# Optimization experiments

Measured on AMD Instinct MI355X. Metric: run time of the kernel, lower is better.

The kernel has to match this reference:

```python
import jax, jax.numpy as jnp
import numpy as np

B, N_L, N_T, C_IN, HID, NG, ATOMS, N_EDGES = 8, 128, 512, 128, 128, 10, 24, 4096
BN_EPS = 1e-5


def setup_inputs() -> dict:
    key = jax.random.key(0)
    ks = jax.random.split(key, 20)
    f32 = jnp.float32
    s = 0.05  # weight scale
    return {
        "h_l_x": jax.random.normal(ks[0], (B, N_L, C_IN), f32),
        "h_t_x": jax.random.normal(ks[1], (B, N_T, C_IN), f32),
        "l_mask": jnp.ones((B, N_L), dtype=bool),
        "t_mask": jnp.ones((B, N_T), dtype=bool),
        "h_l_pos": jax.random.normal(ks[2], (B, N_L, 3), f32),
        "h_t_pos": jax.random.normal(ks[3], (B, N_T * ATOMS, 3), f32),
        "x_l_flat": jax.random.normal(ks[4], (B * N_L, C_IN), f32),
        "edge_index": jax.random.randint(ks[5], (2, N_EDGES), 0, B * N_L),
        "W1": jax.random.normal(ks[6], (2 * C_IN, HID), f32) * s,
        "b1": jnp.zeros((HID,), f32),
        "bn_gamma": jnp.ones((HID,), f32),
        "bn_beta": jnp.zeros((HID,), f32),
        "bn_mean": jnp.zeros((HID,), f32),
        "bn_var": jnp.ones((HID,), f32),
        "W_pi": jax.random.normal(ks[7], (HID, NG), f32) * s,
        "b_pi": jnp.zeros((NG,), f32),
        "W_sigma": jax.random.normal(ks[8], (HID, NG), f32) * s,
        "b_sigma": jnp.zeros((NG,), f32),
        "W_mu": jax.random.normal(ks[9], (HID, NG), f32) * s,
        "b_mu": jnp.zeros((NG,), f32),
        "W_nuc": jax.random.normal(ks[10], (C_IN, 12), f32) * s,
        "b_nuc": jnp.zeros((12,), f32),
        "W_bond": jax.random.normal(ks[11], (2 * C_IN, 4), f32) * s,
        "b_bond": jnp.zeros((4,), f32),
    }


def reference(h_l_x, h_t_x, l_mask, t_mask, h_l_pos, h_t_pos, x_l_flat, edge_index,
              W1, b1, bn_gamma, bn_beta, bn_mean, bn_var,
              W_pi, b_pi, W_sigma, b_sigma, W_mu, b_mu,
              W_nuc, b_nuc, W_bond, b_bond):
    Bsz, Nl, Cd = h_l_x.shape
    Nt = h_t_x.shape[1]
    # dense pairwise concat: [B, N_l, N_t, 2C] (masks are all-True, so the
    # boolean selection C[C_mask] of the original is a static flatten)
    pair = jnp.concatenate([
        jnp.broadcast_to(h_l_x[:, :, None, :], (Bsz, Nl, Nt, Cd)),
        jnp.broadcast_to(h_t_x[:, None, :, :], (Bsz, Nl, Nt, Cd)),
    ], axis=-1).reshape(-1, 2 * Cd)
    # MLP: Linear -> BatchNorm1d (eval, running stats) -> ELU -> Dropout(eval=id)
    h = pair @ W1 + b1
    h = (h - bn_mean) * jax.lax.rsqrt(bn_var + BN_EPS) * bn_gamma + bn_beta
    h = jax.nn.elu(h)
    # MDN heads
    pi = jax.nn.softmax(h @ W_pi + b_pi, axis=-1)
    sigma = jax.nn.elu(h @ W_sigma + b_sigma) + 1.1
    mu = jax.nn.elu(h @ W_mu + b_mu) + 1.0
    # auxiliary heads on flat ligand node features
    nuc_types = x_l_flat @ W_nuc + b_nuc
    bond_feat = jnp.concatenate([x_l_flat[edge_index[0]], x_l_flat[edge_index[1]]], axis=1)
    bond_types = bond_feat @ W_bond + b_bond
    # pairwise distances with windowed min over 24 atoms per target residue
    d2 = (-2.0 * jnp.einsum('bld,btd->blt', h_l_pos, h_t_pos)
          + jnp.sum(h_t_pos ** 2, axis=-1)[:, None, :]
          + jnp.sum(h_l_pos ** 2, axis=-1)[:, :, None])
    d = jnp.nan_to_num(jnp.sqrt(d2), nan=10000.0)  # nan from sqrt(<0)
    dist = d.reshape(Bsz, Nl, Nt, ATOMS).min(axis=-1)  # [B, N_l, N_t]
    dist = jax.lax.stop_gradient(dist.reshape(-1)[:, None])  # detached, [M,1]
    C_batch = jnp.broadcast_to(jnp.arange(Bsz)[:, None, None], (Bsz, Nl, Nt)).reshape(-1)
    return (pi, sigma, mu, dist, nuc_types, bond_types, C_batch)
```

## Files before the change

### kernel.cpp

```cpp
#include <hip/hip_runtime.h>

#define B_      8
#define N_L     128
#define N_T     512
#define C_IN    128
#define HID     128
#define NG      10
#define ATOMS   24
#define N_EDGES 4096

#define OFF_PI  0
#define OFF_SG  5242880
#define OFF_MU  10485760
#define OFF_DI  15728640
#define OFF_NU  16252928
#define OFF_BO  16265216
#define OFF_CB  16281600

#define WS_U    0
#define WS_V    131072
#define WS_B    659456
#define WS_WT   659488

typedef unsigned short u16;
typedef unsigned int   u32;
typedef short s16x8 __attribute__((ext_vector_type(8)));
typedef float f32x4 __attribute__((ext_vector_type(4)));
typedef u32   u32x4 __attribute__((ext_vector_type(4)));

__device__ __forceinline__ float bfu2f(u16 s) {
  u32 u = ((u32)s) << 16;
  return __builtin_bit_cast(float, u);
}
__device__ __forceinline__ u16 f2bf(float f) {
  u32 u = __builtin_bit_cast(u32, f);
  u32 r = (u + 0x7fffu + ((u >> 16) & 1u)) >> 16;
  return (u16)r;
}
__device__ __forceinline__ u32 pack2(float a, float b) {
  return (u32)f2bf(a) | ((u32)f2bf(b) << 16);
}
__device__ __forceinline__ u32 pkhi(float hi, float lo) {
  return __builtin_amdgcn_perm(__builtin_bit_cast(u32, hi),
                               __builtin_bit_cast(u32, lo), 0x07060302u);
}
__device__ __forceinline__ float eluf(float x) {
  return x > 0.f ? x : __expf(x) - 1.f;
}
__device__ __forceinline__ s16x8 ld8(const u16* p) {
  return __builtin_bit_cast(s16x8, *(const u32x4*)p);
}

template<bool F32>
__device__ __forceinline__ float ldf(const void* p, size_t i) {
  if constexpr (F32) return ((const float*)p)[i];
  else               return bfu2f(((const u16*)p)[i]);
}
template<bool F32>
__device__ __forceinline__ u16 wraw(const void* p, size_t i) {
  if constexpr (F32) return f2bf(((const float*)p)[i]);
  else               return ((const u16*)p)[i];
}
__device__ __forceinline__ bool is_f32(const u32* probe) {
  return (probe[0] & 0xFFFFu) == 0u;
}

template<bool F32>
__device__ __forceinline__ void prep_rows(
    int blk, int tid,
    const void* hlx, const void* htx, const void* W1, const void* b1,
    const void* gam, const void* bet, const void* mean_, const void* var_,
    float* __restrict__ ws, float (*xs)[C_IN]) {
  int k = tid & 127, g = tid >> 7;
  bool isU = (blk < 128);
  const void* x = isU ? hlx : htx;
  int row0 = isU ? blk * 8 : (blk - 128) * 8;
  size_t woff = isU ? 0 : (size_t)C_IN * HID;
  #pragma unroll
  for (int i = 0; i < 4; ++i) {
    int e = tid + i * 256;
    int rr = e >> 7, cc = e & 127;
    xs[rr][cc] = ldf<F32>(x, (size_t)(row0 + rr) * C_IN + cc);
  }
  __syncthreads();
  float a0 = 0.f, a1 = 0.f, a2 = 0.f, a3 = 0.f;
  const float* xr0 = xs[g * 4 + 0];
  const float* xr1 = xs[g * 4 + 1];
  const float* xr2 = xs[g * 4 + 2];
  const float* xr3 = xs[g * 4 + 3];
  #pragma unroll 8
  for (int c = 0; c < C_IN; ++c) {
    float w = ldf<F32>(W1, woff + (size_t)c * HID + k);
    a0 += xr0[c] * w;
    a1 += xr1[c] * w;
    a2 += xr2[c] * w;
    a3 += xr3[c] * w;
  }
  float A = ldf<F32>(gam, k) * rsqrtf(ldf<F32>(var_, k) + 1e-5f);
  float add = 0.f;
  if (isU) add = ldf<F32>(b1, k) * A + (ldf<F32>(bet, k) - ldf<F32>(mean_, k) * A);
  float* dst = ws + (isU ? WS_U : WS_V) + (size_t)row0 * HID;
  dst[(g * 4 + 0) * HID + k] = a0 * A + add;
  dst[(g * 4 + 1) * HID + k] = a1 * A + add;
  dst[(g * 4 + 2) * HID + k] = a2 * A + add;
  dst[(g * 4 + 3) * HID + k] = a3 * A + add;
}

template<bool F32>
__device__ __forceinline__ void prep_consts(
    int tid, const void* Wpi, const void* bpi, const void* Wsg, const void* bsg,
    const void* Wmu, const void* bmu, float* __restrict__ ws) {
  if (tid >= 128) return;
  int k = tid;
  u16* wt = (u16*)(ws + WS_WT);
  for (int j = 0; j < 32; ++j) {
    u16 val = 0;
    if (j < 10)      val = wraw<F32>(Wpi, (size_t)k * NG + j);
    else if (j < 20) val = wraw<F32>(Wsg, (size_t)k * NG + j - 10);
    else if (j < 30) val = wraw<F32>(Wmu, (size_t)k * NG + j - 20);
    wt[(size_t)j * HID + k] = val;
  }
  if (k < 32) {
    float bb = 0.f;
    if (k < 10)      bb = ldf<F32>(bpi, k);
    else if (k < 20) bb = ldf<F32>(bsg, k - 10);
    else if (k < 30) bb = ldf<F32>(bmu, k - 20);
    ws[WS_B + k] = bb;
  }
}

template<bool F32>
__device__ __forceinline__ void dist_impl(int blk2,
                                          const void* __restrict__ lpos,
                                          const void* __restrict__ tpos,
                                          void* __restrict__ out) {
  int lc   = blk2 & 63;
  int half = (blk2 >> 6) & 1;
  int b    = blk2 >> 7;
  int t = half * 256 + threadIdx.x;

  size_t tbase = ((size_t)b * (N_T * ATOMS) + (size_t)t * ATOMS) * 3;
  float ax[ATOMS], ay[ATOMS], az[ATOMS], an[ATOMS];
  if constexpr (F32) {
    float c[72];
    const float4* tp4 = (const float4*)((const float*)tpos + tbase);
    #pragma unroll
    for (int i = 0; i < 18; ++i) {
      float4 qv = tp4[i];
      c[4*i+0] = qv.x; c[4*i+1] = qv.y; c[4*i+2] = qv.z; c[4*i+3] = qv.w;
    }
    #pragma unroll
    for (int a = 0; a < ATOMS; ++a) {
      ax[a] = c[3*a]; ay[a] = c[3*a+1]; az[a] = c[3*a+2];
      an[a] = ax[a]*ax[a] + ay[a]*ay[a] + az[a]*az[a];
    }
  } else {
    u32 raw[36];
    const uint4* tp4 = (const uint4*)((const u16*)tpos + tbase);
    #pragma unroll
    for (int i = 0; i < 9; ++i) {
      uint4 qv = tp4[i];
      raw[4*i+0] = qv.x; raw[4*i+1] = qv.y; raw[4*i+2] = qv.z; raw[4*i+3] = qv.w;
    }
    #pragma unroll
    for (int a = 0; a < ATOMS; ++a) {
      int e = 3 * a;
      u32 w0 = raw[e >> 1];
      ax[a] = bfu2f((e & 1) ? (u16)(w0 >> 16) : (u16)w0);
      u32 w1 = raw[(e + 1) >> 1];
      ay[a] = bfu2f(((e + 1) & 1) ? (u16)(w1 >> 16) : (u16)w1);
      u32 w2 = raw[(e + 2) >> 1];
      az[a] = bfu2f(((e + 2) & 1) ? (u16)(w2 >> 16) : (u16)w2);
      an[a] = ax[a]*ax[a] + ay[a]*ay[a] + az[a]*az[a];
    }
  }
  #pragma unroll
  for (int il = 0; il < 2; ++il) {
    int l = lc * 2 + il;
    size_t lbase = ((size_t)b * N_L + l) * 3;
    float lx = ldf<F32>(lpos, lbase), ly = ldf<F32>(lpos, lbase+1), lz = ldf<F32>(lpos, lbase+2);
    float ln = lx*lx + ly*ly + lz*lz;
    float m = 1e30f;
    #pragma unroll
    for (int a = 0; a < ATOMS; ++a) {
      float dot = ax[a]*lx + ay[a]*ly + az[a]*lz;
      float d2 = ln + an[a] - 2.f * dot;
      d2 = (d2 >= 0.f) ? d2 : 1e30f;
      m = fminf(m, d2);
    }
    float d = (m < 1e29f) ? sqrtf(m) : 10000.0f;
    long p = ((long)(b * N_L + l)) * N_T + t;
    if constexpr (F32) {
      ((float*)out)[OFF_DI + p] = d;
      ((float*)out)[OFF_CB + p] = (float)b;
    } else {
      ((u16*)out)[OFF_DI + p] = f2bf(d);
      ((u16*)out)[OFF_CB + p] = f2bf((float)b);
    }
  }
}

__global__ __launch_bounds__(256) void prep_fused(
    const void* hlx, const void* htx, const void* W1, const void* b1,
    const void* gam, const void* bet, const void* mean_, const void* var_,
    const void* Wpi, const void* bpi, const void* Wsg, const void* bsg,
    const void* Wmu, const void* bmu, float* ws,
    const void* lpos, const void* tpos, void* out, const u32* probe) {
  __shared__ float xs[8][C_IN];
  int blk = blockIdx.x;
  int tid = threadIdx.x;
  bool f = is_f32(probe);
  if (blk < 640) {
    if (f) prep_rows<true >(blk, tid, hlx, htx, W1, b1, gam, bet, mean_, var_, ws, xs);
    else   prep_rows<false>(blk, tid, hlx, htx, W1, b1, gam, bet, mean_, var_, ws, xs);
  } else if (blk == 640) {
    if (f) prep_consts<true >(tid, Wpi, bpi, Wsg, bsg, Wmu, bmu, ws);
    else   prep_consts<false>(tid, Wpi, bpi, Wsg, bsg, Wmu, bmu, ws);
  } else {
    int blk2 = blk - 641;
    if (f) dist_impl<true >(blk2, lpos, tpos, out);
    else   dist_impl<false>(blk2, lpos, tpos, out);
  }
}

template<bool F32>
__device__ __forceinline__ void nuc_wave(int r, int lane, const void* __restrict__ xl,
    const void* __restrict__ Wnu, const void* __restrict__ bnu, void* __restrict__ out) {
  float x0 = ldf<F32>(xl, (size_t)r * C_IN + lane);
  float x1 = ldf<F32>(xl, (size_t)r * C_IN + 64 + lane);
  #pragma unroll
  for (int j = 0; j < 12; ++j) {
    float a = x0 * ldf<F32>(Wnu, (size_t)lane * 12 + j)
            + x1 * ldf<F32>(Wnu, (size_t)(64 + lane) * 12 + j);
    #pragma unroll
    for (int m = 32; m >= 1; m >>= 1) a += __shfl_xor(a, m);
    if (lane == 0) {
      float v = a + ldf<F32>(bnu, j);
      if constexpr (F32) ((float*)out)[OFF_NU + (size_t)r * 12 + j] = v;
      else               ((u16*)out)[OFF_NU + (size_t)r * 12 + j] = f2bf(v);
    }
  }
}

template<bool F32>
__device__ __forceinline__ void bond_wave(int e, int lane, const void* __restrict__ xl,
    const int* __restrict__ eidx, const void* __restrict__ Wbo,
    const void* __restrict__ bbo, void* __restrict__ out) {
  int e0 = eidx[e], e1 = eidx[N_EDGES + e];
  float x0 = ldf<F32>(xl, (size_t)e0 * C_IN + lane);
  float x1 = ldf<F32>(xl, (size_t)e0 * C_IN + 64 + lane);
  float y0 = ldf<F32>(xl, (size_t)e1 * C_IN + lane);
  float y1 = ldf<F32>(xl, (size_t)e1 * C_IN + 64 + lane);
  #pragma unroll
  for (int j = 0; j < 4; ++j) {
    float a = x0 * ldf<F32>(Wbo, (size_t)lane * 4 + j)
            + x1 * ldf<F32>(Wbo, (size_t)(64 + lane) * 4 + j)
            + y0 * ldf<F32>(Wbo, (size_t)(128 + lane) * 4 + j)
            + y1 * ldf<F32>(Wbo, (size_t)(192 + lane) * 4 + j);
    #pragma unroll
    for (int m = 32; m >= 1; m >>= 1) a += __shfl_xor(a, m);
    if (lane == 0) {
      float v = a + ldf<F32>(bbo, j);
      if constexpr (F32) ((float*)out)[OFF_BO + (size_t)e * 4 + j] = v;
      else               ((u16*)out)[OFF_BO + (size_t)e * 4 + j] = f2bf(v);
    }
  }
}

__global__ __launch_bounds__(256, 4) void main_fused(
    const float* __restrict__ ws, void* __restrict__ out, const u32* probe,
    const void* __restrict__ xl, const int* __restrict__ eidx,
    const void* __restrict__ Wnu, const void* __restrict__ bnu,
    const void* __restrict__ Wbo, const void* __restrict__ bbo) {
  int blk = blockIdx.x;
  int tid = threadIdx.x;
  int lane = tid & 63, wave = tid >> 6;
  bool f32o = is_f32(probe);

  if (blk >= 1024) {
    if (blk < 1024 + 256) {
      int r = (blk - 1024) * 4 + wave;
      if (f32o) nuc_wave<true >(r, lane, xl, Wnu, bnu, out);
      else      nuc_wave<false>(r, lane, xl, Wnu, bnu, out);
    } else {
      int e = (blk - 1280) * 4 + wave;
      if (f32o) bond_wave<true >(e, lane, xl, eidx, Wbo, bbo, out);
      else      bond_wave<false>(e, lane, xl, eidx, Wbo, bbo, out);
    }
    return;
  }

  int p = lane & 15, q = lane >> 4;
  int bl = blk;
  int b = bl >> 7;

  const u16* wt = (const u16*)(ws + WS_WT);
  s16x8 wf0[4], wf1[4];
  #pragma unroll
  for (int kt = 0; kt < 4; ++kt) {
    wf0[kt] = ld8(wt + (size_t)p        * HID + kt*32 + q*8);
    wf1[kt] = ld8(wt + (size_t)(16 + p) * HID + kt*32 + q*8);
  }
  const float* up = ws + WS_U + (size_t)bl * HID;
  float ue[4][8];
  #pragma unroll
  for (int kt = 0; kt < 4; ++kt) {
    f32x4 a0 = *(const f32x4*)(up + kt*32 + q*8);
    f32x4 a1 = *(const f32x4*)(up + kt*32 + q*8 + 4);
    #pragma unroll
    for (int i = 0; i < 4; ++i) { ue[kt][i] = a0[i]; ue[kt][4+i] = a1[i]; }
  }
  float bias0[4], bias1[4];
  #pragma unroll
  for (int r = 0; r < 4; ++r) {
    bias0[r] = ws[WS_B + q*4 + r];
    bias1[r] = ws[WS_B + 16 + q*4 + r];
  }

  #pragma unroll 1
  for (int tc = 0; tc < 4; ++tc) {
    #pragma unroll
    for (int tt = 0; tt < 2; ++tt) {
      int t = tc * 128 + wave * 32 + tt * 16 + p;
      const float* vp = ws + WS_V + (size_t)(b * N_T + t) * HID;
      f32x4 acc0 = {0.f,0.f,0.f,0.f}, acc1 = {0.f,0.f,0.f,0.f};
      #pragma unroll
      for (int kt = 0; kt < 4; ++kt) {
        f32x4 va = *(const f32x4*)(vp + kt*32 + q*8);
        f32x4 vb = *(const f32x4*)(vp + kt*32 + q*8 + 4);
        float h0 = eluf(va[0] + ue[kt][0]);
        float h1 = eluf(va[1] + ue[kt][1]);
        float h2 = eluf(va[2] + ue[kt][2]);
        float h3 = eluf(va[3] + ue[kt][3]);
        float h4 = eluf(vb[0] + ue[kt][4]);
        float h5 = eluf(vb[1] + ue[kt][5]);
        float h6 = eluf(vb[2] + ue[kt][6]);
        float h7 = eluf(vb[3] + ue[kt][7]);
        u32x4 hw = { pkhi(h1,h0), pkhi(h3,h2), pkhi(h5,h4), pkhi(h7,h6) };
        s16x8 hf = __builtin_bit_cast(s16x8, hw);
        acc0 = __builtin_amdgcn_mfma_f32_16x16x32_bf16(wf0[kt], hf, acc0, 0, 0, 0);
        acc1 = __builtin_amdgcn_mfma_f32_16x16x32_bf16(wf1[kt], hf, acc1, 0, 0, 0);
      }
      float v0[4], v1[4];
      #pragma unroll
      for (int r = 0; r < 4; ++r) { v0[r] = acc0[r] + bias0[r]; v1[r] = acc1[r] + bias1[r]; }
      float pm = -3.0e38f;
      #pragma unroll
      for (int r = 0; r < 4; ++r) if (q*4 + r < 10) pm = fmaxf(pm, v0[r]);
      pm = fmaxf(pm, __shfl_xor(pm, 16));
      pm = fmaxf(pm, __shfl_xor(pm, 32));
      float e[4]; float es = 0.f;
      #pragma unroll
      for (int r = 0; r < 4; ++r) {
        e[r] = 0.f;
        if (q*4 + r < 10) { e[r] = __expf(v0[r] - pm); es += e[r]; }
      }
      es += __shfl_xor(es, 16);
      es += __shfl_xor(es, 32);
      float inv = 1.f / es;
      size_t base = ((size_t)bl * N_T + t) * NG;

      if (f32o) {
        float* o = (float*)out;
        if (q == 0) {
          *(float2*)(o + OFF_PI + base + 0) = make_float2(e[0]*inv, e[1]*inv);
          *(float2*)(o + OFF_PI + base + 2) = make_float2(e[2]*inv, e[3]*inv);
          *(float2*)(o + OFF_SG + base + 6) = make_float2(eluf(v1[0])+1.1f, eluf(v1[1])+1.1f);
          *(float2*)(o + OFF_SG + base + 8) = make_float2(eluf(v1[2])+1.1f, eluf(v1[3])+1.1f);
        } else if (q == 1) {
          *(float2*)(o + OFF_PI + base + 4) = make_float2(e[0]*inv, e[1]*inv);
          *(float2*)(o + OFF_PI + base + 6) = make_float2(e[2]*inv, e[3]*inv);
          *(float2*)(o + OFF_MU + base + 0) = make_float2(eluf(v1[0])+1.0f, eluf(v1[1])+1.0f);
          *(float2*)(o + OFF_MU + base + 2) = make_float2(eluf(v1[2])+1.0f, eluf(v1[3])+1.0f);
        } else if (q == 2) {
          *(float2*)(o + OFF_PI + base + 8) = make_float2(e[0]*inv, e[1]*inv);
          *(float2*)(o + OFF_SG + base + 0) = make_float2(eluf(v0[2])+1.1f, eluf(v0[3])+1.1f);
          *(float2*)(o + OFF_MU + base + 4) = make_float2(eluf(v1[0])+1.0f, eluf(v1[1])+1.0f);
          *(float2*)(o + OFF_MU + base + 6) = make_float2(eluf(v1[2])+1.0f, eluf(v1[3])+1.0f);
        } else {
          *(float2*)(o + OFF_SG + base + 2) = make_float2(eluf(v0[0])+1.1f, eluf(v0[1])+1.1f);
          *(float2*)(o + OFF_SG + base + 4) = make_float2(eluf(v0[2])+1.1f, eluf(v0[3])+1.1f);
          *(float2*)(o + OFF_MU + base + 8) = make_float2(eluf(v1[0])+1.0f, eluf(v1[1])+1.0f);
        }
      } else {
        u16* o = (u16*)out;
        if (q == 0) {
          *(u32*)(o + OFF_PI + base + 0) = pack2(e[0]*inv, e[1]*inv);
          *(u32*)(o + OFF_PI + base + 2) = pack2(e[2]*inv, e[3]*inv);
          *(u32*)(o + OFF_SG + base + 6) = pack2(eluf(v1[0])+1.1f, eluf(v1[1])+1.1f);
          *(u32*)(o + OFF_SG + base + 8) = pack2(eluf(v1[2])+1.1f, eluf(v1[3])+1.1f);
        } else if (q == 1) {
          *(u32*)(o + OFF_PI + base + 4) = pack2(e[0]*inv, e[1]*inv);
          *(u32*)(o + OFF_PI + base + 6) = pack2(e[2]*inv, e[3]*inv);
          *(u32*)(o + OFF_MU + base + 0) = pack2(eluf(v1[0])+1.0f, eluf(v1[1])+1.0f);
          *(u32*)(o + OFF_MU + base + 2) = pack2(eluf(v1[2])+1.0f, eluf(v1[3])+1.0f);
        } else if (q == 2) {
          *(u32*)(o + OFF_PI + base + 8) = pack2(e[0]*inv, e[1]*inv);
          *(u32*)(o + OFF_SG + base + 0) = pack2(eluf(v0[2])+1.1f, eluf(v0[3])+1.1f);
          *(u32*)(o + OFF_MU + base + 4) = pack2(eluf(v1[0])+1.0f, eluf(v1[1])+1.0f);
          *(u32*)(o + OFF_MU + base + 6) = pack2(eluf(v1[2])+1.0f, eluf(v1[3])+1.0f);
        } else {
          *(u32*)(o + OFF_SG + base + 2) = pack2(eluf(v0[0])+1.1f, eluf(v0[1])+1.1f);
          *(u32*)(o + OFF_SG + base + 4) = pack2(eluf(v0[2])+1.1f, eluf(v0[3])+1.1f);
          *(u32*)(o + OFF_MU + base + 8) = pack2(eluf(v1[0])+1.0f, eluf(v1[1])+1.0f);
        }
      }
    }
  }
}

extern "C" void kernel_launch(void* const* d_in, const int* in_sizes, int n_in,
                              void* d_out, int out_size, void* d_ws, size_t ws_size,
                              hipStream_t stream) {
  int s = (n_in >= 24) ? 2 : 0;
  const void* hlx  = d_in[0];
  const void* htx  = d_in[1];
  const void* lpos = d_in[2 + s];
  const void* tpos = d_in[3 + s];
  const void* xl   = d_in[4 + s];
  const int*  eidx = (const int*)d_in[5 + s];
  const void* W1   = d_in[6 + s];
  const void* b1   = d_in[7 + s];
  const void* gam  = d_in[8 + s];
  const void* bet  = d_in[9 + s];
  const void* mean_= d_in[10 + s];
  const void* var_ = d_in[11 + s];
  const void* Wpi  = d_in[12 + s];
  const void* bpi  = d_in[13 + s];
  const void* Wsg  = d_in[14 + s];
  const void* bsg  = d_in[15 + s];
  const void* Wmu  = d_in[16 + s];
  const void* bmu  = d_in[17 + s];
  const void* Wnu  = d_in[18 + s];
  const void* bnu  = d_in[19 + s];
  const void* Wbo  = d_in[20 + s];
  const void* bbo  = d_in[21 + s];
  const u32* probe = (const u32*)var_;
  float* ws = (float*)d_ws;

  prep_fused<<<1665, 256, 0, stream>>>(hlx, htx, W1, b1, gam, bet, mean_, var_,
                                       Wpi, bpi, Wsg, bsg, Wmu, bmu, ws,
                                       lpos, tpos, d_out, probe);
  main_fused<<<2304, 256, 0, stream>>>(ws, d_out, probe,
                                       xl, eidx, Wnu, bnu, Wbo, bbo);
}
```

Measured before the change: 179.8 us.

## Switch head GEMM to 32x32x16 MFMA with bias-initialized accumulators and LDS u-vector

Replaces the two 16x16x32 bf16 MFMAs per 16-row tile with a single 32x32x16 bf16 MFMA chain covering 32 targets per wave-iteration, so each wave handles 32 t values per step instead of two 16-row subtiles. The bias is preloaded into the accumulator, removing the post-MFMA bias adds. The per-row u vector is staged in LDS once per block rather than held as 32 registers per lane. Output lane-to-column mapping and masking of the softmax are rewritten for the new accumulator layout, which risks layout bugs and adds a __syncthreads and LDS reads per k-step.

```diff
diff --git a/kernel.cpp b/kernel.cpp
--- a/kernel.cpp
+++ b/kernel.cpp
@@ -26,6 +26,7 @@
 typedef unsigned int   u32;
 typedef short s16x8 __attribute__((ext_vector_type(8)));
 typedef float f32x4 __attribute__((ext_vector_type(4)));
+typedef float f32x16 __attribute__((ext_vector_type(16)));
 typedef u32   u32x4 __attribute__((ext_vector_type(4)));
 
 __device__ __forceinline__ float bfu2f(u16 s) {
@@ -272,6 +273,7 @@
     const void* __restrict__ xl, const int* __restrict__ eidx,
     const void* __restrict__ Wnu, const void* __restrict__ bnu,
     const void* __restrict__ Wbo, const void* __restrict__ bbo) {
+  __shared__ float u_lds[C_IN];
   int blk = blockIdx.x;
   int tid = threadIdx.x;
   int lane = tid & 63, wave = tid >> 6;
@@ -290,120 +292,110 @@
     return;
   }
 
-  int p = lane & 15, q = lane >> 4;
   int bl = blk;
-  int b = bl >> 7;
+  int b  = bl >> 7;
+  int j  = lane & 31;
+  int hi = lane >> 5;
+
+  if (tid < C_IN) u_lds[tid] = ws[WS_U + (size_t)bl * HID + tid];
+  __syncthreads();
 
   const u16* wt = (const u16*)(ws + WS_WT);
-  s16x8 wf0[4], wf1[4];
-  #pragma unroll
-  for (int kt = 0; kt < 4; ++kt) {
-    wf0[kt] = ld8(wt + (size_t)p        * HID + kt*32 + q*8);
-    wf1[kt] = ld8(wt + (size_t)(16 + p) * HID + kt*32 + q*8);
-  }
-  const float* up = ws + WS_U + (size_t)bl * HID;
-  float ue[4][8];
-  #pragma unroll
-  for (int kt = 0; kt < 4; ++kt) {
-    f32x4 a0 = *(const f32x4*)(up + kt*32 + q*8);
-    f32x4 a1 = *(const f32x4*)(up + kt*32 + q*8 + 4);
-    #pragma unroll
-    for (int i = 0; i < 4; ++i) { ue[kt][i] = a0[i]; ue[kt][4+i] = a1[i]; }
-  }
-  float bias0[4], bias1[4];
-  #pragma unroll
-  for (int r = 0; r < 4; ++r) {
-    bias0[r] = ws[WS_B + q*4 + r];
-    bias1[r] = ws[WS_B + 16 + q*4 + r];
-  }
+  s16x8 wf[8];
+  #pragma unroll
+  for (int ks = 0; ks < 8; ++ks)
+    wf[ks] = ld8(wt + (size_t)j * HID + ks * 16 + hi * 8);
+
+  float binit[16];
+  #pragma unroll
+  for (int r = 0; r < 16; ++r)
+    binit[r] = ws[WS_B + ((r & 3) + 8 * (r >> 2) + 4 * hi)];
+
+  const float* vbase = ws + WS_V + (size_t)b * N_T * HID;
 
   #pragma unroll 1
-  for (int tc = 0; tc < 4; ++tc) {
-    #pragma unroll
-    for (int tt = 0; tt < 2; ++tt) {
-      int t = tc * 128 + wave * 32 + tt * 16 + p;
-      const float* vp = ws + WS_V + (size_t)(b * N_T + t) * HID;
-      f32x4 acc0 = {0.f,0.f,0.f,0.f}, acc1 = {0.f,0.f,0.f,0.f};
-      #pragma unroll
-      for (int kt = 0; kt < 4; ++kt) {
-        f32x4 va = *(const f32x4*)(vp + kt*32 + q*8);
-        f32x4 vb = *(const f32x4*)(vp + kt*32 + q*8 + 4);
-        float h0 = eluf(va[0] + ue[kt][0]);
-        float h1 = eluf(va[1] + ue[kt][1]);
-        float h2 = eluf(va[2] + ue[kt][2]);
-        float h3 = eluf(va[3] + ue[kt][3]);
-        float h4 = eluf(vb[0] + ue[kt][4]);
-        float h5 = eluf(vb[1] + ue[kt][5]);
-        float h6 = eluf(vb[2] + ue[kt][6]);
-        float h7 = eluf(vb[3] + ue[kt][7]);
-        u32x4 hw = { pkhi(h1,h0), pkhi(h3,h2), pkhi(h5,h4), pkhi(h7,h6) };
-        s16x8 hf = __builtin_bit_cast(s16x8, hw);
-        acc0 = __builtin_amdgcn_mfma_f32_16x16x32_bf16(wf0[kt], hf, acc0, 0, 0, 0);
-        acc1 = __builtin_amdgcn_mfma_f32_16x16x32_bf16(wf1[kt], hf, acc1, 0, 0, 0);
+  for (int it = 0; it < 4; ++it) {
+    int t = it * 128 + wave * 32 + j;
+    const float* vp = vbase + (size_t)t * HID;
+
+    f32x16 acc;
+    #pragma unroll
+    for (int r = 0; r < 16; ++r) acc[r] = binit[r];
+
+    #pragma unroll
+    for (int ks = 0; ks < 8; ++ks) {
+      int ko = ks * 16 + hi * 8;
+      f32x4 va = *(const f32x4*)(vp + ko);
+      f32x4 vb = *(const f32x4*)(vp + ko + 4);
+      f32x4 ua = *(const f32x4*)(u_lds + ko);
+      f32x4 ub = *(const f32x4*)(u_lds + ko + 4);
+      float h0 = eluf(va[0] + ua[0]);
+      float h1 = eluf(va[1] + ua[1]);
+      float h2 = eluf(va[2] + ua[2]);
+      float h3 = eluf(va[3] + ua[3]);
+      float h4 = eluf(vb[0] + ub[0]);
+      float h5 = eluf(vb[1] + ub[1]);
+      float h6 = eluf(vb[2] + ub[2]);
+      float h7 = eluf(vb[3] + ub[3]);
+      u32x4 hw = { pkhi(h1,h0), pkhi(h3,h2), pkhi(h5,h4), pkhi(h7,h6) };
+      s16x8 hf = __builtin_bit_cast(s16x8, hw);
+      acc = __builtin_amdgcn_mfma_f32_32x32x16_bf16(wf[ks], hf, acc, 0, 0, 0);
+    }
+
+    float pm = fmaxf(fmaxf(acc[0], acc[1]), fmaxf(acc[2], acc[3]));
+    if (hi == 0) pm = fmaxf(pm, fmaxf(acc[4], acc[5]));
+    pm = fmaxf(pm, __shfl_xor(pm, 32));
+    float e0 = __expf(acc[0] - pm), e1 = __expf(acc[1] - pm);
+    float e2 = __expf(acc[2] - pm), e3 = __expf(acc[3] - pm);
+    float e4 = 0.f, e5 = 0.f;
+    float es = e0 + e1 + e2 + e3;
+    if (hi == 0) {
+      e4 = __expf(acc[4] - pm); e5 = __expf(acc[5] - pm);
+      es += e4 + e5;
+    }
+    es += __shfl_xor(es, 32);
+    float inv = 1.f / es;
+
+    size_t base = ((size_t)bl * N_T + t) * NG;
+    if (f32o) {
+      float* o = (float*)out;
+      if (hi == 0) {
+        *(float2*)(o + OFF_PI + base + 0) = make_float2(e0*inv, e1*inv);
+        *(float2*)(o + OFF_PI + base + 2) = make_float2(e2*inv, e3*inv);
+        *(float2*)(o + OFF_PI + base + 8) = make_float2(e4*inv, e5*inv);
+        *(float2*)(o + OFF_SG + base + 0) = make_float2(eluf(acc[6])+1.1f,  eluf(acc[7])+1.1f);
+        *(float2*)(o + OFF_SG + base + 6) = make_float2(eluf(acc[8])+1.1f,  eluf(acc[9])+1.1f);
+        *(float2*)(o + OFF_SG + base + 8) = make_float2(eluf(acc[10])+1.1f, eluf(acc[11])+1.1f);
+        *(float2*)(o + OFF_MU + base + 4) = make_float2(eluf(acc[12])+1.0f, eluf(acc[13])+1.0f);
+        *(float2*)(o + OFF_MU + base + 6) = make_float2(eluf(acc[14])+1.0f, eluf(acc[15])+1.0f);
+      } else {
+        *(float2*)(o + OFF_PI + base + 4) = make_float2(e0*inv, e1*inv);
+        *(float2*)(o + OFF_PI + base + 6) = make_float2(e2*inv, e3*inv);
+        *(float2*)(o + OFF_SG + base + 2) = make_float2(eluf(acc[4])+1.1f,  eluf(acc[5])+1.1f);
+        *(float2*)(o + OFF_SG + base + 4) = make_float2(eluf(acc[6])+1.1f,  eluf(acc[7])+1.1f);
+        *(float2*)(o + OFF_MU + base + 0) = make_float2(eluf(acc[8])+1.0f,  eluf(acc[9])+1.0f);
+        *(float2*)(o + OFF_MU + base + 2) = make_float2(eluf(acc[10])+1.0f, eluf(acc[11])+1.0f);
+        *(float2*)(o + OFF_MU + base + 8) = make_float2(eluf(acc[12])+1.0f, eluf(acc[13])+1.0f);
       }
-      float v0[4], v1[4];
-      #pragma unroll
-      for (int r = 0; r < 4; ++r) { v0[r] = acc0[r] + bias0[r]; v1[r] = acc1[r] + bias1[r]; }
-      float pm = -3.0e38f;
-      #pragma unroll
-      for (int r = 0; r < 4; ++r) if (q*4 + r < 10) pm = fmaxf(pm, v0[r]);
-      pm = fmaxf(pm, __shfl_xor(pm, 16));
-      pm = fmaxf(pm, __shfl_xor(pm, 32));
-      float e[4]; float es = 0.f;
-      #pragma unroll
-      for (int r = 0; r < 4; ++r) {
-        e[r] = 0.f;
-        if (q*4 + r < 10) { e[r] = __expf(v0[r] - pm); es += e[r]; }
-      }
-      es += __shfl_xor(es, 16);
-      es += __shfl_xor(es, 32);
-      float inv = 1.f / es;
-      size_t base = ((size_t)bl * N_T + t) * NG;
-
-      if (f32o) {
-        float* o = (float*)out;
-        if (q == 0) {
-          *(float2*)(o + OFF_PI + base + 0) = make_float2(e[0]*inv, e[1]*inv);
-          *(float2*)(o + OFF_PI + base + 2) = make_float2(e[2]*inv, e[3]*inv);
-          *(float2*)(o + OFF_SG + base + 6) = make_float2(eluf(v1[0])+1.1f, eluf(v1[1])+1.1f);
-          *(float2*)(o + OFF_SG + base + 8) = make_float2(eluf(v1[2])+1.1f, eluf(v1[3])+1.1f);
-        } else if (q == 1) {
-          *(float2*)(o + OFF_PI + base + 4) = make_float2(e[0]*inv, e[1]*inv);
-          *(float2*)(o + OFF_PI + base + 6) = make_float2(e[2]*inv, e[3]*inv);
-          *(float2*)(o + OFF_MU + base + 0) = make_float2(eluf(v1[0])+1.0f, eluf(v1[1])+1.0f);
-          *(float2*)(o + OFF_MU + base + 2) = make_float2(eluf(v1[2])+1.0f, eluf(v1[3])+1.0f);
-        } else if (q == 2) {
-          *(float2*)(o + OFF_PI + base + 8) = make_float2(e[0]*inv, e[1]*inv);
-          *(float2*)(o + OFF_SG + base + 0) = make_float2(eluf(v0[2])+1.1f, eluf(v0[3])+1.1f);
-          *(float2*)(o + OFF_MU + base + 4) = make_float2(eluf(v1[0])+1.0f, eluf(v1[1])+1.0f);
-          *(float2*)(o + OFF_MU + base + 6) = make_float2(eluf(v1[2])+1.0f, eluf(v1[3])+1.0f);
-        } else {
-          *(float2*)(o + OFF_SG + base + 2) = make_float2(eluf(v0[0])+1.1f, eluf(v0[1])+1.1f);
-          *(float2*)(o + OFF_SG + base + 4) = make_float2(eluf(v0[2])+1.1f, eluf(v0[3])+1.1f);
-          *(float2*)(o + OFF_MU + base + 8) = make_float2(eluf(v1[0])+1.0f, eluf(v1[1])+1.0f);
-        }
+    } else {
+      u16* o = (u16*)out;
+      if (hi == 0) {
+        *(u32*)(o + OFF_PI + base + 0) = pack2(e0*inv, e1*inv);
+        *(u32*)(o + OFF_PI + base + 2) = pack2(e2*inv, e3*inv);
+        *(u32*)(o + OFF_PI + base + 8) = pack2(e4*inv, e5*inv);
+        *(u32*)(o + OFF_SG + base + 0) = pack2(eluf(acc[6])+1.1f,  eluf(acc[7])+1.1f);
+        *(u32*)(o + OFF_SG + base + 6) = pack2(eluf(acc[8])+1.1f,  eluf(acc[9])+1.1f);
+        *(u32*)(o + OFF_SG + base + 8) = pack2(eluf(acc[10])+1.1f, eluf(acc[11])+1.1f);
+        *(u32*)(o + OFF_MU + base + 4) = pack2(eluf(acc[12])+1.0f, eluf(acc[13])+1.0f);
+        *(u32*)(o + OFF_MU + base + 6) = pack2(eluf(acc[14])+1.0f, eluf(acc[15])+1.0f);
       } else {
-        u16* o = (u16*)out;
-        if (q == 0) {
-          *(u32*)(o + OFF_PI + base + 0) = pack2(e[0]*inv, e[1]*inv);
-          *(u32*)(o + OFF_PI + base + 2) = pack2(e[2]*inv, e[3]*inv);
-          *(u32*)(o + OFF_SG + base + 6) = pack2(eluf(v1[0])+1.1f, eluf(v1[1])+1.1f);
-          *(u32*)(o + OFF_SG + base + 8) = pack2(eluf(v1[2])+1.1f, eluf(v1[3])+1.1f);
-        } else if (q == 1) {
-          *(u32*)(o + OFF_PI + base + 4) = pack2(e[0]*inv, e[1]*inv);
-          *(u32*)(o + OFF_PI + base + 6) = pack2(e[2]*inv, e[3]*inv);
-          *(u32*)(o + OFF_MU + base + 0) = pack2(eluf(v1[0])+1.0f, eluf(v1[1])+1.0f);
-          *(u32*)(o + OFF_MU + base + 2) = pack2(eluf(v1[2])+1.0f, eluf(v1[3])+1.0f);
-        } else if (q == 2) {
-          *(u32*)(o + OFF_PI + base + 8) = pack2(e[0]*inv, e[1]*inv);
-          *(u32*)(o + OFF_SG + base + 0) = pack2(eluf(v0[2])+1.1f, eluf(v0[3])+1.1f);
-          *(u32*)(o + OFF_MU + base + 4) = pack2(eluf(v1[0])+1.0f, eluf(v1[1])+1.0f);
-          *(u32*)(o + OFF_MU + base + 6) = pack2(eluf(v1[2])+1.0f, eluf(v1[3])+1.0f);
-        } else {
-          *(u32*)(o + OFF_SG + base + 2) = pack2(eluf(v0[0])+1.1f, eluf(v0[1])+1.1f);
-          *(u32*)(o + OFF_SG + base + 4) = pack2(eluf(v0[2])+1.1f, eluf(v0[3])+1.1f);
-          *(u32*)(o + OFF_MU + base + 8) = pack2(eluf(v1[0])+1.0f, eluf(v1[1])+1.0f);
-        }
+        *(u32*)(o + OFF_PI + base + 4) = pack2(e0*inv, e1*inv);
+        *(u32*)(o + OFF_PI + base + 6) = pack2(e2*inv, e3*inv);
+        *(u32*)(o + OFF_SG + base + 2) = pack2(eluf(acc[4])+1.1f,  eluf(acc[5])+1.1f);
+        *(u32*)(o + OFF_SG + base + 4) = pack2(eluf(acc[6])+1.1f,  eluf(acc[7])+1.1f);
+        *(u32*)(o + OFF_MU + base + 0) = pack2(eluf(acc[8])+1.0f,  eluf(acc[9])+1.0f);
+        *(u32*)(o + OFF_MU + base + 2) = pack2(eluf(acc[10])+1.0f, eluf(acc[11])+1.0f);
+        *(u32*)(o + OFF_MU + base + 8) = pack2(eluf(acc[12])+1.0f, eluf(acc[13])+1.0f);
       }
     }
   }
```

Measured after the change: 191.6 us. +6.5%, slower.
